# Performance work log

Hardware: AMD Instinct MI355X
Metric: run time of the kernel (lower is better)

## Reference

```python
import jax, jax.numpy as jnp
import numpy as np

R = 64  # all tensor-ring ranks equal

def setup_inputs() -> dict:
    key = jax.random.key(0)
    k1, k2, k3 = jax.random.split(key, 3)
    B, T, N, M, C = 512, 64, 512, 64, 100
    # xavier-uniform-ish scale for weights (gain=init_value=1.0)
    s_sh = float(np.sqrt(6.0 / (R * N + R)))
    s_la = float(np.sqrt(6.0 / (C * R * M + R)))
    return {
        "tensor": jax.random.normal(k1, (B, T, N), dtype=jnp.float32),
        "W_shared": jax.random.uniform(k2, (R, N, R), dtype=jnp.float32, minval=-s_sh, maxval=s_sh),
        "W_last": jax.random.uniform(k3, (C, R, M, R), dtype=jnp.float32, minval=-s_la, maxval=s_la),
    }

def reference(tensor, W_shared, W_last):
    B = tensor.shape[0]
    xt = jnp.transpose(tensor, (1, 0, 2))  # [T, B, N]
    state0 = jnp.ones((R, B, R), dtype=tensor.dtype)  # [r1, B, r2]
    # per-step: x = einsum('bj,rbi->rbji'); state = einsum('ijk,rbji->rbk')
    # == einsum('bj,rbi,ijk->rbk'); factored to avoid the [r,b,n,r] intermediate
    def step(state, x_t):
        bik = jnp.einsum('bj,ijk->bik', x_t, W_shared)   # [B, r2, r3]
        new = jnp.einsum('rbi,bik->rbk', state, bik)     # [r1, B, r3]
        return new, None
    state, _ = jax.lax.scan(step, state0, xt)
    # last kernel with pad_input = ones(B, m):
    # einsum('cijk,rbji->cbrk') with x[r,b,j,i]=state[r,b,i] == sum over j of W_last
    W_sum = jnp.sum(W_last, axis=2)                      # [C, r2, r_last]
    state = jnp.einsum('cik,rbi->cbrk', W_sum, state)    # [C, B, r1, r_last]
    # trace over the last two (square) rank dims
    out = jnp.einsum('cbrr->cb', state)                  # [C, B]
    return out
```

## Files before the change

kernel.cpp:

```cpp
#include <hip/hip_runtime.h>
#include <hip/hip_fp16.h>


typedef _Float16 f16;
typedef __attribute__((ext_vector_type(8))) _Float16 f16x8;
typedef __attribute__((ext_vector_type(2))) _Float16 f16x2;
typedef __attribute__((ext_vector_type(4))) float f32x4;

#define GLDS16(g, l)                                                      \
    __builtin_amdgcn_global_load_lds(                                     \
        (const __attribute__((address_space(1))) void*)(g),               \
        (__attribute__((address_space(3))) void*)(l), 16, 0, 0)

#define BARRIER() asm volatile("s_barrier" ::: "memory")
#define VMCNT(n) asm volatile("s_waitcnt vmcnt(" #n ")" ::: "memory")

__global__ __launch_bounds__(256) void k_usum(const float* __restrict__ Wl,
                                              float* __restrict__ u) {
    int ci = blockIdx.x;
    const float4* p = (const float4*)(Wl + (size_t)ci * 4096);
    int tid = threadIdx.x;
    float s = 0.f;
#pragma unroll
    for (int q = 0; q < 4; ++q) {
        float4 v = p[tid + 256 * q];
        s += v.x + v.y + v.z + v.w;
    }
    __shared__ float red[256];
    red[tid] = s;
    __syncthreads();
    if (tid < 128) red[tid] += red[tid + 128];
    __syncthreads();
    if (tid < 64) {
        float x = red[tid] + red[tid + 64];
#pragma unroll
        for (int off = 32; off > 0; off >>= 1) x += __shfl_down(x, off, 64);
        if (tid == 0) u[ci] = x;
    }
}

__global__ __launch_bounds__(256) void k_prep(const float* __restrict__ tensor,
                                              const float* __restrict__ Wsh,
                                              const float* __restrict__ Wl,
                                              f16* __restrict__ Af16,
                                              f16* __restrict__ Btw,
                                              float* __restrict__ u) {
    __shared__ float red[256];
    int blk = blockIdx.x;
    int tid = threadIdx.x;
    if (blk < 8192) {
        int idx = blk * 256 + tid;
        const float4* p = (const float4*)tensor + (size_t)idx * 2;
        float4 v0 = p[0], v1 = p[1];
        f16x8 h;
        h[0] = (f16)v0.x; h[1] = (f16)v0.y; h[2] = (f16)v0.z; h[3] = (f16)v0.w;
        h[4] = (f16)v1.x; h[5] = (f16)v1.y; h[6] = (f16)v1.z; h[7] = (f16)v1.w;
        *(f16x8*)(Af16 + (size_t)idx * 8) = h;
    } else if (blk < 12288) {
        int o = (blk - 8192) * 256 + tid;
        int col = o >> 8;
        int j = (o & 255) << 1;
        int i = col >> 6, k = col & 63;
        const float* src = Wsh + ((size_t)i * 512 + j) * 64 + k;
        f16x2 pk;
        pk[0] = (f16)src[0];
        pk[1] = (f16)src[64];
        *(f16x2*)(Btw + (size_t)col * 512 + j) = pk;
    } else {
        int ci = blk - 12288;
        const float4* p = (const float4*)(Wl + (size_t)ci * 4096);
        float s = 0.f;
#pragma unroll
        for (int q = 0; q < 4; ++q) {
            float4 v = p[tid + 256 * q];
            s += v.x + v.y + v.z + v.w;
        }
        red[tid] = s;
        __syncthreads();
        if (tid < 128) red[tid] += red[tid + 128];
        __syncthreads();
        if (tid < 64) {
            float x = red[tid] + red[tid + 64];
#pragma unroll
            for (int off = 32; off > 0; off >>= 1) x += __shfl_down(x, off, 64);
            if (tid == 0) u[ci] = x;
        }
    }
}


#define STAGE_A(qq, ha, ktv) do {                                             \
    _Pragma("unroll") for (int u_ = 0; u_ < 2; ++u_) {                        \
        int idx_ = (wid * 2 + u_) * 64 + lane;                                \
        int r_ = idx_ >> 3;                                                   \
        int ls_ = (idx_ & 7) ^ (r_ & 7);                                      \
        const f16* g_ = A + (size_t)(m0 + (ha) * 128 + r_) * 512              \
                          + (ktv) * 64 + ls_ * 8;                             \
        char* l_ = smem + (qq) * 65536 + (ha) * 16384 + (wid * 2 + u_) * 1024;\
        GLDS16(g_, l_);                                                       \
    } } while (0)

#define STAGE_B(qq, hb, ktv) do {                                             \
    _Pragma("unroll") for (int u_ = 0; u_ < 2; ++u_) {                        \
        int idx_ = (wid * 2 + u_) * 64 + lane;                                \
        int r_ = idx_ >> 3;                                                   \
        int ls_ = (idx_ & 7) ^ (r_ & 7);                                      \
        const f16* g_ = Bt + (size_t)(n0 + (hb) * 128 + r_) * 512             \
                           + (ktv) * 64 + ls_ * 8;                            \
        char* l_ = smem + (qq) * 65536 + 32768 + (hb) * 16384                 \
                        + (wid * 2 + u_) * 1024;                              \
        GLDS16(g_, l_);                                                       \
    } } while (0)

#define RD_A(ha, ktv) do {                                                    \
    _Pragma("unroll") for (int mf_ = 0; mf_ < 4; ++mf_)                       \
    _Pragma("unroll") for (int kq_ = 0; kq_ < 2; ++kq_) {                     \
        int ra_ = wr * 64 + mf_ * 16 + (lane & 15);                           \
        int off_ = ((ra_ << 7) + kq_ * 64 + ((lane >> 4) << 4))               \
                   ^ ((ra_ & 7) << 4);                                        \
        a[mf_][kq_] = *(const f16x8*)(smem + ((ktv) & 1) * 65536              \
                                      + (ha) * 16384 + off_);                 \
    } } while (0)

#define RD_B(hb, ktv, breg) do {                                              \
    _Pragma("unroll") for (int nf_ = 0; nf_ < 2; ++nf_)                       \
    _Pragma("unroll") for (int kq_ = 0; kq_ < 2; ++kq_) {                     \
        int rb_ = wc * 32 + nf_ * 16 + (lane & 15);                           \
        int off_ = ((rb_ << 7) + kq_ * 64 + ((lane >> 4) << 4))               \
                   ^ ((rb_ & 7) << 4);                                        \
        breg[nf_][kq_] = *(const f16x8*)(smem + ((ktv) & 1) * 65536           \
                                         + 32768 + (hb) * 16384 + off_);      \
    } } while (0)

#define MFMA_Q(qa_, qb_, breg) do {                                           \
    __builtin_amdgcn_s_setprio(1);                                            \
    _Pragma("unroll") for (int mf_ = 0; mf_ < 4; ++mf_)                       \
    _Pragma("unroll") for (int nf_ = 0; nf_ < 2; ++nf_)                       \
    _Pragma("unroll") for (int kq_ = 0; kq_ < 2; ++kq_)                       \
        acc[qa_][qb_][mf_][nf_] = __builtin_amdgcn_mfma_f32_16x16x32_f16(     \
            a[mf_][kq_], breg[nf_][kq_], acc[qa_][qb_][mf_][nf_], 0, 0, 0);   \
    __builtin_amdgcn_s_setprio(0);                                            \
    } while (0)

__global__ __launch_bounds__(512) void k_gemm_256(const f16* __restrict__ A,
                                                  const f16* __restrict__ Bt,
                                                  __half* __restrict__ outp) {
    extern __shared__ char smem[];
    const int tid = threadIdx.x;
    const int lane = tid & 63;
    const int wid = tid >> 6;
    int lin = blockIdx.x;
    int swz = (lin & 7) * 256 + (lin >> 3);
    const int n0 = (swz & 15) * 256;
    const int m0 = (swz >> 4) * 256;
    const int wr = wid >> 2, wc = wid & 3;

    f32x4 acc[2][2][4][2];
#pragma unroll
    for (int x = 0; x < 2; ++x)
#pragma unroll
        for (int y = 0; y < 2; ++y)
#pragma unroll
            for (int z = 0; z < 4; ++z)
#pragma unroll
                for (int w = 0; w < 2; ++w) acc[x][y][z][w] = (f32x4)0.f;

    f16x8 a[4][2], b0[2][2], b1[2][2];

    STAGE_A(0, 0, 0);
    STAGE_B(0, 0, 0);
    STAGE_B(0, 1, 0);
    STAGE_A(0, 1, 0);
    STAGE_A(1, 0, 1);
    STAGE_B(1, 0, 1);
    STAGE_B(1, 1, 1);

    for (int kt = 0; kt < 6; ++kt) {
        VMCNT(6);
        BARRIER();
        RD_A(0, kt);
        RD_B(0, kt, b0);
        STAGE_A((kt + 1) & 1, 1, kt + 1);
        MFMA_Q(0, 0, b0);
        BARRIER();
        RD_B(1, kt, b1);
        MFMA_Q(0, 1, b1);
        BARRIER();
        RD_A(1, kt);
        STAGE_A(kt & 1, 0, kt + 2);
        STAGE_B(kt & 1, 0, kt + 2);
        MFMA_Q(1, 0, b0);
        BARRIER();
        STAGE_B(kt & 1, 1, kt + 2);
        MFMA_Q(1, 1, b1);
        BARRIER();
    }
    {
        VMCNT(6);
        BARRIER();
        RD_A(0, 6);
        RD_B(0, 6, b0);
        STAGE_A(1, 1, 7);
        MFMA_Q(0, 0, b0);
        BARRIER();
        RD_B(1, 6, b1);
        MFMA_Q(0, 1, b1);
        BARRIER();
        RD_A(1, 6);
        MFMA_Q(1, 0, b0);
        BARRIER();
        MFMA_Q(1, 1, b1);
        BARRIER();
    }
    {
        VMCNT(0);
        BARRIER();
        RD_A(0, 7);
        RD_B(0, 7, b0);
        MFMA_Q(0, 0, b0);
        BARRIER();
        RD_B(1, 7, b1);
        MFMA_Q(0, 1, b1);
        BARRIER();
        RD_A(1, 7);
        MFMA_Q(1, 0, b0);
        BARRIER();
        MFMA_Q(1, 1, b1);
        BARRIER();
    }

    __half* Cs = (__half*)smem;
#pragma unroll
    for (int qa = 0; qa < 2; ++qa)
#pragma unroll
        for (int qb = 0; qb < 2; ++qb)
#pragma unroll
            for (int mf = 0; mf < 4; ++mf)
#pragma unroll
                for (int nf = 0; nf < 2; ++nf)
#pragma unroll
                    for (int j = 0; j < 4; ++j) {
                        int row = qa * 128 + wr * 64 + mf * 16 + ((lane >> 4) << 2) + j;
                        int col = qb * 128 + wc * 32 + nf * 16 + (lane & 15);
                        Cs[row * 256 + col] = __float2half(acc[qa][qb][mf][nf][j]);
                    }
    BARRIER();
#pragma unroll
    for (int it = 0; it < 16; ++it) {
        int idx = it * 512 + tid;
        int r = idx >> 5, seg = idx & 31;
        __builtin_nontemporal_store(
            *(const f32x4*)(Cs + r * 256 + seg * 8),
            (f32x4*)(outp + (size_t)(m0 + r) * 4096 + n0 + seg * 8));
    }
}

#define BM 128
#define BN 64
#define BK 32
__global__ __launch_bounds__(256) void k_gemm(const float* __restrict__ A,
                                              const float* __restrict__ W,
                                              __half* __restrict__ out,
                                              int a_off, int a_stride) {
    __shared__ float As[BK * BM];
    __shared__ float Bs[BK * BN];
    int i0 = blockIdx.x;
    int m0 = blockIdx.y * BM;
    int tid = threadIdx.x;
    int tx = tid & 15, ty = tid >> 4;
    float acc[8][4];
#pragma unroll
    for (int q = 0; q < 8; ++q)
#pragma unroll
        for (int c = 0; c < 4; ++c) acc[q][c] = 0.f;
    const float* wbase = W + (size_t)i0 * 32768;
    for (int j0 = 0; j0 < 512; j0 += BK) {
        {
            int c4 = tid & 7;
            int r = tid >> 3;
#pragma unroll
            for (int p = 0; p < 4; ++p) {
                int row = r + 32 * p;
                float4 v = *(const float4*)(A + (size_t)a_off +
                                            (size_t)(m0 + row) * a_stride + j0 + 4 * c4);
                As[(4 * c4 + 0) * BM + row] = v.x;
                As[(4 * c4 + 1) * BM + row] = v.y;
                As[(4 * c4 + 2) * BM + row] = v.z;
                As[(4 * c4 + 3) * BM + row] = v.w;
            }
            const float4* src = (const float4*)(wbase + (size_t)j0 * 64);
            float4* dst = (float4*)Bs;
            dst[tid] = src[tid];
            dst[tid + 256] = src[tid + 256];
        }
        __syncthreads();
#pragma unroll
        for (int kk = 0; kk < BK; ++kk) {
            float bv[4], av[8];
#pragma unroll
            for (int c = 0; c < 4; ++c) bv[c] = Bs[kk * BN + 4 * tx + c];
#pragma unroll
            for (int q = 0; q < 8; ++q) av[q] = As[kk * BM + 8 * ty + q];
#pragma unroll
            for (int q = 0; q < 8; ++q)
#pragma unroll
                for (int c = 0; c < 4; ++c) acc[q][c] += av[q] * bv[c];
        }
        __syncthreads();
    }
#pragma unroll
    for (int q = 0; q < 8; ++q) {
        int m = m0 + 8 * ty + q;
        __half* o = out + (size_t)m * 4096 + i0 * 64 + 4 * tx;
#pragma unroll
        for (int c = 0; c < 4; ++c) o[c] = __float2half(acc[q][c]);
    }
}

__global__ __launch_bounds__(256) void k_scan(const __half* __restrict__ bik,
                                              const float* __restrict__ u,
                                              float* __restrict__ out) {
    __shared__ char sm[2][8192];
    __shared__ float vsh[64];
    __shared__ float part[256];
    int b = blockIdx.x;
    int tid = threadIdx.x;
    int k = tid & 63, grp = tid >> 6;
    const int lane = tid & 63;
    const int wid = tid >> 6;
    if (tid < 64) vsh[tid] = 1.0f;
    const char* base = (const char*)(bik + (size_t)b * 64 * 4096);

#pragma unroll
    for (int u_ = 0; u_ < 2; ++u_) {
        const char* g = base + (wid * 2 + u_) * 1024 + lane * 16;
        GLDS16(g, &sm[0][0] + (wid * 2 + u_) * 1024);
    }

    for (int t = 0; t < 64; ++t) {
        VMCNT(0);
        __syncthreads();
        if (t < 63) {
            const char* gb = base + (size_t)(t + 1) * 8192;
#pragma unroll
            for (int u_ = 0; u_ < 2; ++u_) {
                const char* g = gb + (wid * 2 + u_) * 1024 + lane * 16;
                GLDS16(g, &sm[(t + 1) & 1][0] + (wid * 2 + u_) * 1024);
            }
        }
        const __half* Mt = (const __half*)&sm[t & 1][0];
        float s = 0.f;
#pragma unroll
        for (int q = 0; q < 16; ++q) {
            int i = grp * 16 + q;
            s += vsh[i] * __half2float(Mt[i * 64 + k]);
        }
        part[tid] = s;
        __syncthreads();
        if (tid < 64) vsh[k] = part[k] + part[64 + k] + part[128 + k] + part[192 + k];
        __syncthreads();
    }
    if (tid < 100) {
        const float* uc = u + tid * 64;
        float s = 0.f;
#pragma unroll 8
        for (int i = 0; i < 64; ++i) s += uc[i] * vsh[i];
        out[tid * 512 + b] = s;
    }
}

__global__ __launch_bounds__(256) void k_update(const __half* __restrict__ Mt,
                                                const float* __restrict__ vin,
                                                float* __restrict__ vout, int first) {
    int o = blockIdx.x * 256 + threadIdx.x;
    int b = o >> 6, k = o & 63;
    const __half* m = Mt + (size_t)b * 4096;
    float s = 0.f;
    if (first) {
#pragma unroll 8
        for (int i = 0; i < 64; ++i) s += __half2float(m[i * 64 + k]);
    } else {
        const float* v = vin + (size_t)b * 64;
#pragma unroll 8
        for (int i = 0; i < 64; ++i) s += v[i] * __half2float(m[i * 64 + k]);
    }
    vout[o] = s;
}

__global__ __launch_bounds__(256) void k_final(const float* __restrict__ u,
                                               const float* __restrict__ v,
                                               float* __restrict__ out) {
    int o = blockIdx.x * 256 + threadIdx.x;
    int c = o >> 9, b = o & 511;
    const float* uc = u + c * 64;
    const float* vb = v + (size_t)b * 64;
    float s = 0.f;
#pragma unroll 8
    for (int i = 0; i < 64; ++i) s += uc[i] * vb[i];
    out[o] = s;
}

extern "C" void kernel_launch(void* const* d_in, const int* in_sizes, int n_in,
                              void* d_out, int out_size, void* d_ws, size_t ws_size,
                              hipStream_t stream) {
    const float* tensor = (const float*)d_in[0];
    const float* Wsh = (const float*)d_in[1];
    const float* Wl = (const float*)d_in[2];
    float* out = (float*)d_out;
    char* ws = (char*)d_ws;

    const size_t bik_bytes = (size_t)32768 * 4096 * sizeof(__half);
    const size_t fast_bytes = bik_bytes + (512u << 10) + ((size_t)16777216 * 2) + ((size_t)4096 * 512 * 2);

    if (ws_size >= fast_bytes) {
        __half* bik = (__half*)ws;
        float* u = (float*)(ws + bik_bytes);
        f16* Af16 = (f16*)(ws + bik_bytes + (512u << 10));
        f16* Btw = Af16 + (size_t)16777216;

        k_prep<<<18688, 256, 0, stream>>>(tensor, Wsh, Wl, Af16, Btw, u);
        (void)hipFuncSetAttribute((const void*)k_gemm_256,
                                  hipFuncAttributeMaxDynamicSharedMemorySize, 131072);
        k_gemm_256<<<2048, 512, 131072, stream>>>(Af16, Btw, bik);
        k_scan<<<512, 256, 0, stream>>>(bik, u, out);
    } else if (ws_size >= bik_bytes + (2u << 20)) {
        __half* bik = (__half*)ws;
        float* u = (float*)(ws + bik_bytes);

        k_usum<<<6400, 256, 0, stream>>>(Wl, u);
        dim3 g(64, 256);
        k_gemm<<<g, 256, 0, stream>>>(tensor, Wsh, bik, 0, 512);
        k_scan<<<512, 256, 0, stream>>>(bik, u, out);
    } else {
        __half* bikt = (__half*)ws;
        float* u = (float*)(ws + (size_t)(4 << 20));
        float* v0 = (float*)(ws + (size_t)(4 << 20) + (64 << 10));
        float* v1 = v0 + 32768;

        k_usum<<<6400, 256, 0, stream>>>(Wl, u);
        for (int t = 0; t < 64; ++t) {
            dim3 g(64, 4);
            k_gemm<<<g, 256, 0, stream>>>(tensor, Wsh, bikt, t * 512, 32768);
            float* vin = (t & 1) ? v0 : v1;
            float* vout = (t & 1) ? v1 : v0;
            k_update<<<128, 256, 0, stream>>>(bikt, (t == 0) ? v0 : vin, vout, t == 0);
        }
        k_final<<<200, 256, 0, stream>>>(u, v1, out);
    }
}
```

Measured before the change: 265.6 us.

## Split GEMM and scan into two time chunks to keep intermediate cache-resident

The per-step bik tensor is produced in two halves of 32 time steps each instead of all 64 at once. Each half is consumed by a scan pass that carries the state vector through global memory between passes. The intent is that the smaller 128MB intermediate stays in the large last-level cache, and the GEMM stores become ordinary rather than nontemporal so the data is kept there. The scan also moves to a triple-buffered prefetch with one barrier less per step. The cost is an extra pair of kernel launches and a state round trip through global memory.

```diff
diff --git a/kernel.cpp b/kernel.cpp
--- a/kernel.cpp
+++ b/kernel.cpp
@@ -94,7 +94,8 @@
         int idx_ = (wid * 2 + u_) * 64 + lane;                                \
         int r_ = idx_ >> 3;                                                   \
         int ls_ = (idx_ & 7) ^ (r_ & 7);                                      \
-        const f16* g_ = A + (size_t)(m0 + (ha) * 128 + r_) * 512              \
+        int gr_ = m0 + (ha) * 128 + r_;                                       \
+        const f16* g_ = A + (size_t)((gr_ >> 5) * 64 + t0 + (gr_ & 31)) * 512 \
                           + (ktv) * 64 + ls_ * 8;                             \
         char* l_ = smem + (qq) * 65536 + (ha) * 16384 + (wid * 2 + u_) * 1024;\
         GLDS16(g_, l_);                                                       \
@@ -144,13 +145,14 @@
 
 __global__ __launch_bounds__(512) void k_gemm_256(const f16* __restrict__ A,
                                                   const f16* __restrict__ Bt,
-                                                  __half* __restrict__ outp) {
+                                                  __half* __restrict__ outp,
+                                                  int t0) {
     extern __shared__ char smem[];
     const int tid = threadIdx.x;
     const int lane = tid & 63;
     const int wid = tid >> 6;
     int lin = blockIdx.x;
-    int swz = (lin & 7) * 256 + (lin >> 3);
+    int swz = (lin & 7) * 128 + (lin >> 3);
     const int n0 = (swz & 15) * 256;
     const int m0 = (swz >> 4) * 256;
     const int wr = wid >> 2, wc = wid & 3;
@@ -249,9 +251,8 @@
     for (int it = 0; it < 16; ++it) {
         int idx = it * 512 + tid;
         int r = idx >> 5, seg = idx & 31;
-        __builtin_nontemporal_store(
-            *(const f32x4*)(Cs + r * 256 + seg * 8),
-            (f32x4*)(outp + (size_t)(m0 + r) * 4096 + n0 + seg * 8));
+        *(f32x4*)(outp + (size_t)(m0 + r) * 4096 + n0 + seg * 8) =
+            *(const f32x4*)(Cs + r * 256 + seg * 8);
     }
 }
 
@@ -318,9 +319,12 @@
 }
 
 __global__ __launch_bounds__(256) void k_scan(const __half* __restrict__ bik,
+                                              int bstride,
                                               const float* __restrict__ u,
-                                              float* __restrict__ out) {
-    __shared__ char sm[2][8192];
+                                              float* __restrict__ vg,
+                                              float* __restrict__ out,
+                                              int first, int last) {
+    __shared__ char sm[3][8192];
     __shared__ float vsh[64];
     __shared__ float part[256];
     int b = blockIdx.x;
@@ -328,44 +332,58 @@
     int k = tid & 63, grp = tid >> 6;
     const int lane = tid & 63;
     const int wid = tid >> 6;
-    if (tid < 64) vsh[tid] = 1.0f;
-    const char* base = (const char*)(bik + (size_t)b * 64 * 4096);
-
-#pragma unroll
-    for (int u_ = 0; u_ < 2; ++u_) {
-        const char* g = base + (wid * 2 + u_) * 1024 + lane * 16;
-        GLDS16(g, &sm[0][0] + (wid * 2 + u_) * 1024);
-    }
-
-    for (int t = 0; t < 64; ++t) {
+    if (tid < 64) vsh[tid] = first ? 1.0f : vg[b * 64 + tid];
+    const char* base = (const char*)(bik + (size_t)b * bstride * 4096);
+
+#define SCAN_STAGE(tt) do {                                                   \
+    const char* gb_ = base + (size_t)(tt) * 8192;                             \
+    _Pragma("unroll") for (int u_ = 0; u_ < 2; ++u_) {                        \
+        GLDS16(gb_ + (wid * 2 + u_) * 1024 + lane * 16,                       \
+               &sm[(tt) % 3][0] + (wid * 2 + u_) * 1024);                     \
+    } } while (0)
+
+#define SCAN_STEP(bufidx) do {                                                \
+    const __half* Mt_ = (const __half*)&sm[bufidx][0];                        \
+    float s_ = 0.f;                                                           \
+    _Pragma("unroll") for (int q_ = 0; q_ < 16; ++q_)                         \
+        s_ += vsh[grp * 16 + q_] * __half2float(Mt_[(grp * 16 + q_) * 64 + k]);\
+    part[tid] = s_;                                                           \
+    __syncthreads();                                                          \
+    if (tid < 64)                                                             \
+        vsh[k] = part[k] + part[64 + k] + part[128 + k] + part[192 + k];      \
+    } while (0)
+
+    SCAN_STAGE(0);
+    SCAN_STAGE(1);
+    VMCNT(2);
+    __syncthreads();
+
+    for (int t = 0; t < 30; ++t) {
+        SCAN_STAGE(t + 2);
+        SCAN_STEP(t % 3);
+        VMCNT(2);
+        __syncthreads();
+    }
+    {
+        SCAN_STEP(0);
         VMCNT(0);
         __syncthreads();
-        if (t < 63) {
-            const char* gb = base + (size_t)(t + 1) * 8192;
-#pragma unroll
-            for (int u_ = 0; u_ < 2; ++u_) {
-                const char* g = gb + (wid * 2 + u_) * 1024 + lane * 16;
-                GLDS16(g, &sm[(t + 1) & 1][0] + (wid * 2 + u_) * 1024);
-            }
-        }
-        const __half* Mt = (const __half*)&sm[t & 1][0];
-        float s = 0.f;
-#pragma unroll
-        for (int q = 0; q < 16; ++q) {
-            int i = grp * 16 + q;
-            s += vsh[i] * __half2float(Mt[i * 64 + k]);
-        }
-        part[tid] = s;
-        __syncthreads();
-        if (tid < 64) vsh[k] = part[k] + part[64 + k] + part[128 + k] + part[192 + k];
-        __syncthreads();
-    }
-    if (tid < 100) {
-        const float* uc = u + tid * 64;
-        float s = 0.f;
+    }
+    {
+        SCAN_STEP(1);
+        __syncthreads();
+    }
+
+    if (last) {
+        if (tid < 100) {
+            const float* uc = u + tid * 64;
+            float s = 0.f;
 #pragma unroll 8
-        for (int i = 0; i < 64; ++i) s += uc[i] * vsh[i];
-        out[tid * 512 + b] = s;
+            for (int i = 0; i < 64; ++i) s += uc[i] * vsh[i];
+            out[tid * 512 + b] = s;
+        }
+    } else {
+        if (tid < 64) vg[b * 64 + tid] = vsh[tid];
     }
 }
 
@@ -409,28 +427,35 @@
     float* out = (float*)d_out;
     char* ws = (char*)d_ws;
 
-    const size_t bik_bytes = (size_t)32768 * 4096 * sizeof(__half);
-    const size_t fast_bytes = bik_bytes + (512u << 10) + ((size_t)16777216 * 2) + ((size_t)4096 * 512 * 2);
+    const size_t bik_full = (size_t)32768 * 4096 * sizeof(__half);
+    const size_t bik_chunk = (size_t)16384 * 4096 * sizeof(__half);
+    const size_t fast_bytes = (40u << 20) + bik_chunk;
 
     if (ws_size >= fast_bytes) {
-        __half* bik = (__half*)ws;
-        float* u = (float*)(ws + bik_bytes);
-        f16* Af16 = (f16*)(ws + bik_bytes + (512u << 10));
+        float* u = (float*)ws;
+        float* vg = (float*)(ws + (256u << 10));
+        f16* Af16 = (f16*)(ws + (1u << 20));
         f16* Btw = Af16 + (size_t)16777216;
+        __half* bik_c = (__half*)(ws + (40u << 20));
 
         k_prep<<<18688, 256, 0, stream>>>(tensor, Wsh, Wl, Af16, Btw, u);
         (void)hipFuncSetAttribute((const void*)k_gemm_256,
                                   hipFuncAttributeMaxDynamicSharedMemorySize, 131072);
-        k_gemm_256<<<2048, 512, 131072, stream>>>(Af16, Btw, bik);
-        k_scan<<<512, 256, 0, stream>>>(bik, u, out);
-    } else if (ws_size >= bik_bytes + (2u << 20)) {
+        for (int c = 0; c < 2; ++c) {
+            k_gemm_256<<<1024, 512, 131072, stream>>>(Af16, Btw, bik_c, c * 32);
+            k_scan<<<512, 256, 0, stream>>>(bik_c, 32, u, vg, out, c == 0, c == 1);
+        }
+    } else if (ws_size >= bik_full + (2u << 20)) {
         __half* bik = (__half*)ws;
-        float* u = (float*)(ws + bik_bytes);
+        float* u = (float*)(ws + bik_full);
+        float* vg = (float*)(ws + bik_full + (128u << 10));
 
         k_usum<<<6400, 256, 0, stream>>>(Wl, u);
         dim3 g(64, 256);
         k_gemm<<<g, 256, 0, stream>>>(tensor, Wsh, bik, 0, 512);
-        k_scan<<<512, 256, 0, stream>>>(bik, u, out);
+        for (int c = 0; c < 2; ++c)
+            k_scan<<<512, 256, 0, stream>>>(bik + (size_t)c * 32 * 4096, 64,
+                                            u, vg, out, c == 0, c == 1);
     } else {
         __half* bikt = (__half*)ws;
         float* u = (float*)(ws + (size_t)(4 << 20));
```

Result: no change. 267.4 us (+0.7%).

## Transpose bik layout and run per-wave register-resident scan kernel

Applied to the files above, without the earlier changes.

The weight prep now writes the GEMM B operand with k-major column ordering, so each bik row for a given output k is contiguous across i. A new scan kernel assigns one wave per batch element: each lane loads its 64 contiguous f16 coefficients directly into registers, double-buffered across timesteps, and updates the shared state vector with only wave-level LDS fences instead of block barriers. This removes the LDS staging and __syncthreads per step but halves the thread count per batch and uses many more VGPRs, and it still depends on a serial chain of global loads.

```diff
diff --git a/kernel.cpp b/kernel.cpp
--- a/kernel.cpp
+++ b/kernel.cpp
@@ -14,6 +14,11 @@
 
 #define BARRIER() asm volatile("s_barrier" ::: "memory")
 #define VMCNT(n) asm volatile("s_waitcnt vmcnt(" #n ")" ::: "memory")
+#define WAVE_LDS_FENCE()                                                  \
+    do {                                                                  \
+        asm volatile("s_waitcnt lgkmcnt(0)" ::: "memory");                \
+        __builtin_amdgcn_sched_barrier(0);                                \
+    } while (0)
 
 __global__ __launch_bounds__(256) void k_usum(const float* __restrict__ Wl,
                                               float* __restrict__ u) {
@@ -60,7 +65,7 @@
         int o = (blk - 8192) * 256 + tid;
         int col = o >> 8;
         int j = (o & 255) << 1;
-        int i = col >> 6, k = col & 63;
+        int k = col >> 6, i = col & 63;
         const float* src = Wsh + ((size_t)i * 512 + j) * 64 + k;
         f16x2 pk;
         pk[0] = (f16)src[0];
@@ -87,7 +92,6 @@
         }
     }
 }
-
 
 #define STAGE_A(qq, ha, ktv) do {                                             \
     _Pragma("unroll") for (int u_ = 0; u_ < 2; ++u_) {                        \
@@ -317,6 +321,58 @@
     }
 }
 
+__global__ __launch_bounds__(128) void k_scan_t(const __half* __restrict__ bik,
+                                                const float* __restrict__ u,
+                                                float* __restrict__ out) {
+    __shared__ float vsh[2][64];
+    const int tid = threadIdx.x;
+    const int wid = tid >> 6;
+    const int k = tid & 63;
+    const int b = blockIdx.x * 2 + wid;
+    float* vs = vsh[wid];
+    const f16* row = (const f16*)bik + ((size_t)b * 64) * 4096 + k * 64;
+
+    vs[k] = 1.0f;
+    f16x8 A0[8], A1[8];
+#pragma unroll
+    for (int q = 0; q < 8; ++q) A0[q] = *(const f16x8*)(row + q * 8);
+#pragma unroll
+    for (int q = 0; q < 8; ++q) A1[q] = *(const f16x8*)(row + 4096 + q * 8);
+    WAVE_LDS_FENCE();
+
+#define SCAN_T_STEP(BUF, tnext) do {                                          \
+    float s0 = 0.f, s1 = 0.f, s2 = 0.f, s3 = 0.f;                             \
+    _Pragma("unroll") for (int q_ = 0; q_ < 8; q_ += 4) {                     \
+        _Pragma("unroll") for (int e_ = 0; e_ < 8; ++e_) {                    \
+            s0 += vs[(q_ + 0) * 8 + e_] * (float)BUF[q_ + 0][e_];             \
+            s1 += vs[(q_ + 1) * 8 + e_] * (float)BUF[q_ + 1][e_];             \
+            s2 += vs[(q_ + 2) * 8 + e_] * (float)BUF[q_ + 2][e_];             \
+            s3 += vs[(q_ + 3) * 8 + e_] * (float)BUF[q_ + 3][e_];             \
+        }                                                                     \
+    }                                                                         \
+    if ((tnext) < 64) {                                                       \
+        const f16* r_ = row + (size_t)(tnext) * 4096;                         \
+        _Pragma("unroll") for (int q_ = 0; q_ < 8; ++q_)                      \
+            BUF[q_] = *(const f16x8*)(r_ + q_ * 8);                           \
+    }                                                                         \
+    vs[k] = (s0 + s1) + (s2 + s3);                                            \
+    WAVE_LDS_FENCE();                                                         \
+    } while (0)
+
+    for (int t = 0; t < 64; t += 2) {
+        SCAN_T_STEP(A0, t + 2);
+        SCAN_T_STEP(A1, t + 3);
+    }
+
+    for (int c = k; c < 100; c += 64) {
+        const float* uc = u + c * 64;
+        float s = 0.f;
+#pragma unroll 8
+        for (int i = 0; i < 64; ++i) s += uc[i] * vs[i];
+        out[c * 512 + b] = s;
+    }
+}
+
 __global__ __launch_bounds__(256) void k_scan(const __half* __restrict__ bik,
                                               const float* __restrict__ u,
                                               float* __restrict__ out) {
@@ -330,13 +386,11 @@
     const int wid = tid >> 6;
     if (tid < 64) vsh[tid] = 1.0f;
     const char* base = (const char*)(bik + (size_t)b * 64 * 4096);
-
 #pragma unroll
     for (int u_ = 0; u_ < 2; ++u_) {
         const char* g = base + (wid * 2 + u_) * 1024 + lane * 16;
         GLDS16(g, &sm[0][0] + (wid * 2 + u_) * 1024);
     }
-
     for (int t = 0; t < 64; ++t) {
         VMCNT(0);
         __syncthreads();
@@ -422,7 +476,7 @@
         (void)hipFuncSetAttribute((const void*)k_gemm_256,
                                   hipFuncAttributeMaxDynamicSharedMemorySize, 131072);
         k_gemm_256<<<2048, 512, 131072, stream>>>(Af16, Btw, bik);
-        k_scan<<<512, 256, 0, stream>>>(bik, u, out);
+        k_scan_t<<<256, 128, 0, stream>>>(bik, u, out);
     } else if (ws_size >= bik_bytes + (2u << 20)) {
         __half* bik = (__half*)ws;
         float* u = (float*)(ws + bik_bytes);
```

New measurement: 251.1 us, median of 2. 1.06x faster.
